# Performance work log

Hardware: AMD Instinct MI355X
Metric: run time of the kernel (lower is better)

## Reference

```python
import jax, jax.numpy as jnp
import numpy as np


def setup_inputs() -> dict:
    key = jax.random.key(0)
    bs, width, length = 4, 1536, 2048  # width = 3 * num_heads * ch = 3*8*64
    qkv = jax.random.normal(key, (bs, width, length), dtype=jnp.float32)
    return {"qkv": qkv, "num_heads": 8}


def reference(qkv, num_heads):
    bs, width, length = qkv.shape
    assert width % (3 * num_heads) == 0
    ch = width // (3 * num_heads)
    q, k, v = jnp.split(qkv, 3, axis=1)  # each [bs, num_heads*ch, length]
    scale = 1.0 / np.sqrt(np.sqrt(ch))  # applied to both q and k (total 1/sqrt(ch))
    q = (q * scale).reshape(bs * num_heads, ch, length)
    k = (k * scale).reshape(bs * num_heads, ch, length)
    v = v.reshape(bs * num_heads, ch, length)
    # weight[b, t, s] = sum_c q[b,c,t] * k[b,c,s]
    weight = jnp.einsum('bct,bcs->bts', q, k)
    weight = jax.nn.softmax(weight.astype(jnp.float32), axis=-1).astype(weight.dtype)
    # a[b, c, t] = sum_s weight[b,t,s] * v[b,c,s]
    a = jnp.einsum('bts,bcs->bct', weight, v)
    return a.reshape(bs, num_heads * ch, length)
```

## Files before the change

### kernel.cpp

```cpp
#include <hip/hip_runtime.h>

typedef float f32x16 __attribute__((ext_vector_type(16)));
typedef float f32x2 __attribute__((ext_vector_type(2)));
typedef short short8 __attribute__((ext_vector_type(8)));
typedef unsigned short u16;
typedef unsigned int u32;

#define SEQ_L 2048

#if __has_builtin(__builtin_amdgcn_exp2f)
#define EXP2(x) __builtin_amdgcn_exp2f(x)
#else
#define EXP2(x) exp2f(x)
#endif

__device__ __forceinline__ u32 pk2bf(float lo, float hi) {
#if __has_builtin(__builtin_amdgcn_cvt_pk_bf16_f32)
    typedef __bf16 bf16x2_t __attribute__((ext_vector_type(2)));
    union { bf16x2_t v; u32 i; } w;
    w.v = __builtin_amdgcn_cvt_pk_bf16_f32(lo, hi);
    return w.i;
#else
    union { float f; u32 i; } a, b; a.f = lo; b.f = hi;
    return ((a.i + 0x8000u) >> 16) | ((b.i + 0x8000u) & 0xFFFF0000u);
#endif
}

#define KT_U16 (64 * 64)
#define VT_STRIDE 72
#define VT_U16 (64 * VT_STRIDE)
#define GRP_U16 (KT_U16 + VT_U16)

__global__ __launch_bounds__(512, 4)
void attn_kernel(const float* __restrict__ qkv, float* __restrict__ out) {
    const int tid  = threadIdx.x;
    const int lane = tid & 63;
    const int wv   = tid >> 6;
    const int g    = wv >> 2;
    const int wvin = wv & 3;
    const int col  = lane & 31;
    const int half = lane >> 5;

    const int gid  = blockIdx.x;
    const int head = gid & 31;
    const int tb   = gid >> 5;
    const int t0   = tb * 128 + wvin * 32;
    const int bb   = head >> 3, hh = head & 7;

    const size_t qoff = ((size_t)bb * 1536 + (size_t)hh * 64) * SEQ_L;
    const float* qp = qkv + qoff;
    const float* kp = qp + (size_t)512  * SEQ_L;
    const float* vp = qp + (size_t)1024 * SEQ_L;
    float* op = out + ((size_t)bb * 512 + (size_t)hh * 64) * SEQ_L;

    __shared__ __align__(16) u16 smem[2 * GRP_U16];
    u16* ktg = smem + g * GRP_U16;
    u16* vtg = ktg + KT_U16;

    const int gtid = tid & 255;
    const int sgrp = gtid & 15;
    const int rq   = gtid >> 4;
    const int sbase0 = g * 1024;

    u16* kw[4];
#pragma unroll
    for (int j = 0; j < 4; ++j) {
        int s = 4 * sgrp + j;
        int sw = ((s >> 2) ^ s) & 7;
        kw[j] = ktg + s * 64 + (((rq >> 1) ^ sw) << 3) + ((rq & 1) << 2);
    }
    const int vcoloff = ((sgrp >> 2) << 4) + ((sgrp & 1) << 3) + (((sgrp >> 1) & 1) << 2);
    u16* vw = vtg + rq * VT_STRIDE + vcoloff;

    const int sw_r = ((col >> 2) ^ col) & 7;
    int kco[4];
#pragma unroll
    for (int ks = 0; ks < 4; ++ks) kco[ks] = ((2 * ks + half) ^ sw_r) << 3;
    const u16* krb0 = ktg + col * 64;
    const u16* krb1 = ktg + (32 + col) * 64;
    const u16* vrb0 = vtg + col * VT_STRIDE + half * 8;
    const u16* vrb1 = vtg + (32 + col) * VT_STRIDE + half * 8;

    const int t = t0 + col;
    const float qscale = 0.18033688f;
    short8 qf[4];
#pragma unroll
    for (int ks = 0; ks < 4; ++ks) {
        union { u32 u[4]; short8 v; } qq;
#pragma unroll
        for (int e2 = 0; e2 < 4; ++e2) {
            int c = ks * 16 + half * 8 + 2 * e2;
            qq.u[e2] = pk2bf(qp[(size_t)c * SEQ_L + t] * qscale,
                             qp[(size_t)(c + 1) * SEQ_L + t] * qscale);
        }
        qf[ks] = qq.v;
    }

    f32x16 zacc;
#pragma unroll
    for (int r = 0; r < 16; ++r) zacc[r] = 0.0f;

    f32x16 accO[2];
#pragma unroll
    for (int m = 0; m < 2; ++m)
#pragma unroll
        for (int r = 0; r < 16; ++r) accO[m][r] = 0.0f;
    f32x2 ls2 = {0.0f, 0.0f};

    float4 kreg[4], vreg[4];
#pragma unroll
    for (int rr = 0; rr < 4; ++rr) {
        kreg[rr] = *(const float4*)(kp + (size_t)(4 * rq + rr) * SEQ_L + sbase0 + 4 * sgrp);
        vreg[rr] = *(const float4*)(vp + (size_t)(rq + 16 * rr) * SEQ_L + sbase0 + 4 * sgrp);
    }

    for (int it = 0; it < 16; ++it) {
        __syncthreads();
#pragma unroll
        for (int j = 0; j < 4; ++j) {
            uint2 w;
            w.x = pk2bf(kreg[0][j], kreg[1][j]);
            w.y = pk2bf(kreg[2][j], kreg[3][j]);
            *(uint2*)kw[j] = w;
        }
#pragma unroll
        for (int rr = 0; rr < 4; ++rr) {
            uint2 w;
            w.x = pk2bf(vreg[rr].x, vreg[rr].y);
            w.y = pk2bf(vreg[rr].z, vreg[rr].w);
            *(uint2*)(vw + 16 * rr * VT_STRIDE) = w;
        }
        __syncthreads();

        if (it + 1 < 16) {
            const int sn = sbase0 + (it + 1) * 64;
#pragma unroll
            for (int rr = 0; rr < 4; ++rr) {
                kreg[rr] = *(const float4*)(kp + (size_t)(4 * rq + rr) * SEQ_L + sn + 4 * sgrp);
                vreg[rr] = *(const float4*)(vp + (size_t)(rq + 16 * rr) * SEQ_L + sn + 4 * sgrp);
            }
        }

        f32x16 acc[2];
#pragma unroll
        for (int mb = 0; mb < 2; ++mb) {
            const u16* rb = mb ? krb1 : krb0;
            acc[mb] = __builtin_amdgcn_mfma_f32_32x32x16_bf16(
                *(const short8*)(rb + kco[0]), qf[0], zacc, 0, 0, 0);
#pragma unroll
            for (int ks = 1; ks < 4; ++ks)
                acc[mb] = __builtin_amdgcn_mfma_f32_32x32x16_bf16(
                    *(const short8*)(rb + kco[ks]), qf[ks], acc[mb], 0, 0, 0);
        }

        u32 preg[2][8];
#pragma unroll
        for (int mb = 0; mb < 2; ++mb) {
            f32x2 p2[8];
#pragma unroll
            for (int u2 = 0; u2 < 8; ++u2) {
                float px = EXP2(acc[mb][2 * u2]);
                float py = EXP2(acc[mb][2 * u2 + 1]);
                p2[u2][0] = px; p2[u2][1] = py;
                preg[mb][u2] = pk2bf(px, py);
            }
            f32x2 a0 = p2[0] + p2[1], a1 = p2[2] + p2[3];
            f32x2 a2 = p2[4] + p2[5], a3 = p2[6] + p2[7];
            ls2 += (a0 + a1) + (a2 + a3);
        }

#pragma unroll
        for (int mk = 0; mk < 4; ++mk) {
            int mb = mk >> 1, kb = mk & 1;
            union { u32 u[4]; short8 v; } bfrag;
            bfrag.u[0] = preg[mb][4 * kb + 0];
            bfrag.u[1] = preg[mb][4 * kb + 1];
            bfrag.u[2] = preg[mb][4 * kb + 2];
            bfrag.u[3] = preg[mb][4 * kb + 3];
#pragma unroll
            for (int mbc = 0; mbc < 2; ++mbc) {
                const u16* vb = (mbc ? vrb1 : vrb0) + mk * 16;
                accO[mbc] = __builtin_amdgcn_mfma_f32_32x32x16_bf16(
                    *(const short8*)vb, bfrag.v, accO[mbc], 0, 0, 0);
            }
        }
    }

    float lsum = ls2[0] + ls2[1];

    __syncthreads();
    float* ep = (float*)smem;
    if (g == 1) {
        float* row = ep + (wvin * 64 + lane) * 33;
#pragma unroll
        for (int mbc = 0; mbc < 2; ++mbc)
#pragma unroll
            for (int r = 0; r < 16; ++r) row[mbc * 16 + r] = accO[mbc][r];
        row[32] = lsum;
    }
    __syncthreads();
    if (g == 0) {
        const float* row = ep + (wvin * 64 + lane) * 33;
#pragma unroll
        for (int mbc = 0; mbc < 2; ++mbc)
#pragma unroll
            for (int r = 0; r < 16; ++r) accO[mbc][r] += row[mbc * 16 + r];
        lsum += row[32];
        float ltot = lsum + __shfl_xor(lsum, 32, 64);
        float inv = 1.0f / ltot;
#pragma unroll
        for (int mbc = 0; mbc < 2; ++mbc) {
#pragma unroll
            for (int r = 0; r < 16; ++r) {
                int c = mbc * 32 + (r & 3) + 8 * (r >> 2) + 4 * half;
                op[(size_t)c * SEQ_L + t] = accO[mbc][r] * inv;
            }
        }
    }
}

extern "C" void kernel_launch(void* const* d_in, const int* in_sizes, int n_in,
                              void* d_out, int out_size, void* d_ws, size_t ws_size,
                              hipStream_t stream) {
    (void)in_sizes; (void)n_in; (void)d_ws; (void)ws_size; (void)out_size;
    const float* qkv = (const float*)d_in[0];
    float* out = (float*)d_out;
    attn_kernel<<<dim3(512), dim3(512), 0, stream>>>(qkv, out);
}
```

Measured before the change: 129.3 us.

## Process two 32-query tiles per wave to reuse K/V tiles across queries

Each wave now handles 64 query positions (two 32-column tiles) instead of 32, so every K and V fragment loaded from LDS feeds two MFMAs. The grid halves to 256 blocks, and the bf16 conversion and LDS staging of K/V are amortized over twice as many queries. The cost is roughly double the accumulator registers and a launch bound lowered to 2, which reduces occupancy, and 256 blocks may underfill the GPU's 256 CUs at one block per CU. The epilogue shared buffer is enlarged to hold both tiles' partial results.

```diff
diff --git a/kernel.cpp b/kernel.cpp
--- a/kernel.cpp
+++ b/kernel.cpp
@@ -30,8 +30,9 @@
 #define VT_STRIDE 72
 #define VT_U16 (64 * VT_STRIDE)
 #define GRP_U16 (KT_U16 + VT_U16)
-
-__global__ __launch_bounds__(512, 4)
+#define SMEM_U16 33792
+
+__global__ __launch_bounds__(512, 2)
 void attn_kernel(const float* __restrict__ qkv, float* __restrict__ out) {
     const int tid  = threadIdx.x;
     const int lane = tid & 63;
@@ -44,7 +45,7 @@
     const int gid  = blockIdx.x;
     const int head = gid & 31;
     const int tb   = gid >> 5;
-    const int t0   = tb * 128 + wvin * 32;
+    const int t0   = tb * 256 + wvin * 64;
     const int bb   = head >> 3, hh = head & 7;
 
     const size_t qoff = ((size_t)bb * 1536 + (size_t)hh * 64) * SEQ_L;
@@ -53,7 +54,7 @@
     const float* vp = qp + (size_t)1024 * SEQ_L;
     float* op = out + ((size_t)bb * 512 + (size_t)hh * 64) * SEQ_L;
 
-    __shared__ __align__(16) u16 smem[2 * GRP_U16];
+    __shared__ __align__(16) u16 smem[SMEM_U16];
     u16* ktg = smem + g * GRP_U16;
     u16* vtg = ktg + KT_U16;
 
@@ -81,31 +82,36 @@
     const u16* vrb0 = vtg + col * VT_STRIDE + half * 8;
     const u16* vrb1 = vtg + (32 + col) * VT_STRIDE + half * 8;
 
-    const int t = t0 + col;
+    const int tA = t0 + col;
+    const int tB = tA + 32;
     const float qscale = 0.18033688f;
-    short8 qf[4];
+    short8 qfA[4], qfB[4];
 #pragma unroll
     for (int ks = 0; ks < 4; ++ks) {
-        union { u32 u[4]; short8 v; } qq;
+        union { u32 u[4]; short8 v; } qa, qb;
 #pragma unroll
         for (int e2 = 0; e2 < 4; ++e2) {
             int c = ks * 16 + half * 8 + 2 * e2;
-            qq.u[e2] = pk2bf(qp[(size_t)c * SEQ_L + t] * qscale,
-                             qp[(size_t)(c + 1) * SEQ_L + t] * qscale);
-        }
-        qf[ks] = qq.v;
+            const float* c0 = qp + (size_t)c * SEQ_L;
+            const float* c1 = qp + (size_t)(c + 1) * SEQ_L;
+            qa.u[e2] = pk2bf(c0[tA] * qscale, c1[tA] * qscale);
+            qb.u[e2] = pk2bf(c0[tB] * qscale, c1[tB] * qscale);
+        }
+        qfA[ks] = qa.v; qfB[ks] = qb.v;
     }
 
     f32x16 zacc;
 #pragma unroll
     for (int r = 0; r < 16; ++r) zacc[r] = 0.0f;
 
-    f32x16 accO[2];
-#pragma unroll
-    for (int m = 0; m < 2; ++m)
-#pragma unroll
-        for (int r = 0; r < 16; ++r) accO[m][r] = 0.0f;
-    f32x2 ls2 = {0.0f, 0.0f};
+    f32x16 accO[2][2];
+#pragma unroll
+    for (int tt = 0; tt < 2; ++tt)
+#pragma unroll
+        for (int m = 0; m < 2; ++m)
+#pragma unroll
+            for (int r = 0; r < 16; ++r) accO[tt][m][r] = 0.0f;
+    f32x2 lsA = {0.0f, 0.0f}, lsB = {0.0f, 0.0f};
 
     float4 kreg[4], vreg[4];
 #pragma unroll
@@ -141,79 +147,100 @@
             }
         }
 
-        f32x16 acc[2];
+        f32x16 accA[2], accB[2];
 #pragma unroll
         for (int mb = 0; mb < 2; ++mb) {
             const u16* rb = mb ? krb1 : krb0;
-            acc[mb] = __builtin_amdgcn_mfma_f32_32x32x16_bf16(
-                *(const short8*)(rb + kco[0]), qf[0], zacc, 0, 0, 0);
-#pragma unroll
-            for (int ks = 1; ks < 4; ++ks)
-                acc[mb] = __builtin_amdgcn_mfma_f32_32x32x16_bf16(
-                    *(const short8*)(rb + kco[ks]), qf[ks], acc[mb], 0, 0, 0);
-        }
-
-        u32 preg[2][8];
+            short8 kf0 = *(const short8*)(rb + kco[0]);
+            accA[mb] = __builtin_amdgcn_mfma_f32_32x32x16_bf16(kf0, qfA[0], zacc, 0, 0, 0);
+            accB[mb] = __builtin_amdgcn_mfma_f32_32x32x16_bf16(kf0, qfB[0], zacc, 0, 0, 0);
+#pragma unroll
+            for (int ks = 1; ks < 4; ++ks) {
+                short8 kf = *(const short8*)(rb + kco[ks]);
+                accA[mb] = __builtin_amdgcn_mfma_f32_32x32x16_bf16(kf, qfA[ks], accA[mb], 0, 0, 0);
+                accB[mb] = __builtin_amdgcn_mfma_f32_32x32x16_bf16(kf, qfB[ks], accB[mb], 0, 0, 0);
+            }
+        }
+
+        u32 pregA[2][8], pregB[2][8];
 #pragma unroll
         for (int mb = 0; mb < 2; ++mb) {
-            f32x2 p2[8];
+            f32x2 a2[4], b2[4];
 #pragma unroll
             for (int u2 = 0; u2 < 8; ++u2) {
-                float px = EXP2(acc[mb][2 * u2]);
-                float py = EXP2(acc[mb][2 * u2 + 1]);
-                p2[u2][0] = px; p2[u2][1] = py;
-                preg[mb][u2] = pk2bf(px, py);
-            }
-            f32x2 a0 = p2[0] + p2[1], a1 = p2[2] + p2[3];
-            f32x2 a2 = p2[4] + p2[5], a3 = p2[6] + p2[7];
-            ls2 += (a0 + a1) + (a2 + a3);
+                float ax = EXP2(accA[mb][2 * u2]);
+                float ay = EXP2(accA[mb][2 * u2 + 1]);
+                pregA[mb][u2] = pk2bf(ax, ay);
+                f32x2 av = {ax, ay};
+                if (u2 < 4) a2[u2] = av; else a2[u2 - 4] += av;
+            }
+            lsA += (a2[0] + a2[1]) + (a2[2] + a2[3]);
+#pragma unroll
+            for (int u2 = 0; u2 < 8; ++u2) {
+                float bx = EXP2(accB[mb][2 * u2]);
+                float by = EXP2(accB[mb][2 * u2 + 1]);
+                pregB[mb][u2] = pk2bf(bx, by);
+                f32x2 bv = {bx, by};
+                if (u2 < 4) b2[u2] = bv; else b2[u2 - 4] += bv;
+            }
+            lsB += (b2[0] + b2[1]) + (b2[2] + b2[3]);
         }
 
 #pragma unroll
         for (int mk = 0; mk < 4; ++mk) {
             int mb = mk >> 1, kb = mk & 1;
-            union { u32 u[4]; short8 v; } bfrag;
-            bfrag.u[0] = preg[mb][4 * kb + 0];
-            bfrag.u[1] = preg[mb][4 * kb + 1];
-            bfrag.u[2] = preg[mb][4 * kb + 2];
-            bfrag.u[3] = preg[mb][4 * kb + 3];
+            union { u32 u[4]; short8 v; } bfA, bfB;
+#pragma unroll
+            for (int i = 0; i < 4; ++i) {
+                bfA.u[i] = pregA[mb][4 * kb + i];
+                bfB.u[i] = pregB[mb][4 * kb + i];
+            }
 #pragma unroll
             for (int mbc = 0; mbc < 2; ++mbc) {
-                const u16* vb = (mbc ? vrb1 : vrb0) + mk * 16;
-                accO[mbc] = __builtin_amdgcn_mfma_f32_32x32x16_bf16(
-                    *(const short8*)vb, bfrag.v, accO[mbc], 0, 0, 0);
-            }
-        }
-    }
-
-    float lsum = ls2[0] + ls2[1];
+                short8 vf = *(const short8*)((mbc ? vrb1 : vrb0) + mk * 16);
+                accO[0][mbc] = __builtin_amdgcn_mfma_f32_32x32x16_bf16(vf, bfA.v, accO[0][mbc], 0, 0, 0);
+                accO[1][mbc] = __builtin_amdgcn_mfma_f32_32x32x16_bf16(vf, bfB.v, accO[1][mbc], 0, 0, 0);
+            }
+        }
+    }
+
+    float lsum[2];
+    lsum[0] = lsA[0] + lsA[1];
+    lsum[1] = lsB[0] + lsB[1];
 
     __syncthreads();
     float* ep = (float*)smem;
     if (g == 1) {
-        float* row = ep + (wvin * 64 + lane) * 33;
-#pragma unroll
-        for (int mbc = 0; mbc < 2; ++mbc)
-#pragma unroll
-            for (int r = 0; r < 16; ++r) row[mbc * 16 + r] = accO[mbc][r];
-        row[32] = lsum;
+#pragma unroll
+        for (int tt = 0; tt < 2; ++tt) {
+            float* row = ep + ((wvin * 64 + lane) * 2 + tt) * 33;
+#pragma unroll
+            for (int mbc = 0; mbc < 2; ++mbc)
+#pragma unroll
+                for (int r = 0; r < 16; ++r) row[mbc * 16 + r] = accO[tt][mbc][r];
+            row[32] = lsum[tt];
+        }
     }
     __syncthreads();
     if (g == 0) {
-        const float* row = ep + (wvin * 64 + lane) * 33;
-#pragma unroll
-        for (int mbc = 0; mbc < 2; ++mbc)
-#pragma unroll
-            for (int r = 0; r < 16; ++r) accO[mbc][r] += row[mbc * 16 + r];
-        lsum += row[32];
-        float ltot = lsum + __shfl_xor(lsum, 32, 64);
-        float inv = 1.0f / ltot;
-#pragma unroll
-        for (int mbc = 0; mbc < 2; ++mbc) {
-#pragma unroll
-            for (int r = 0; r < 16; ++r) {
-                int c = mbc * 32 + (r & 3) + 8 * (r >> 2) + 4 * half;
-                op[(size_t)c * SEQ_L + t] = accO[mbc][r] * inv;
+#pragma unroll
+        for (int tt = 0; tt < 2; ++tt) {
+            const float* row = ep + ((wvin * 64 + lane) * 2 + tt) * 33;
+#pragma unroll
+            for (int mbc = 0; mbc < 2; ++mbc)
+#pragma unroll
+                for (int r = 0; r < 16; ++r) accO[tt][mbc][r] += row[mbc * 16 + r];
+            float lt = lsum[tt] + row[32];
+            float ltot = lt + __shfl_xor(lt, 32, 64);
+            float inv = 1.0f / ltot;
+            const int t = tt ? tB : tA;
+#pragma unroll
+            for (int mbc = 0; mbc < 2; ++mbc) {
+#pragma unroll
+                for (int r = 0; r < 16; ++r) {
+                    int c = mbc * 32 + (r & 3) + 8 * (r >> 2) + 4 * half;
+                    op[(size_t)c * SEQ_L + t] = accO[tt][mbc][r] * inv;
+                }
             }
         }
     }
@@ -225,5 +252,5 @@
     (void)in_sizes; (void)n_in; (void)d_ws; (void)ws_size; (void)out_size;
     const float* qkv = (const float*)d_in[0];
     float* out = (float*)d_out;
-    attn_kernel<<<dim3(512), dim3(512), 0, stream>>>(qkv, out);
+    attn_kernel<<<dim3(256), dim3(512), 0, stream>>>(qkv, out);
 }
```

New measurement: 118.8 us. 8.1% less time.
